# Kernel tuning notes

Hardware: AMD Instinct MI355X
Metric: run time of the kernel (lower is better)

Reference implementation:

```python
import jax, jax.numpy as jnp
import numpy as np

N, D, E, NNZ = 200000, 128, 1024, 1600000


def setup_inputs() -> dict:
    key = jax.random.key(0)
    ks = jax.random.split(key, 8)
    x = jax.random.normal(ks[0], (N, D), jnp.float32)
    tb_W = jax.random.normal(ks[1], (5, 3, D, D), jnp.float32) * 0.05
    tb_b = jax.random.normal(ks[2], (5, 3, D), jnp.float32) * 0.05
    hg_W = jax.random.normal(ks[3], (2, D, D), jnp.float32) * 0.05
    hg_b = jax.random.normal(ks[4], (2, D), jnp.float32) * 0.05
    hyperedge_attr = jax.random.normal(ks[5], (E, D), jnp.float32)
    node_idx = jax.random.randint(ks[6], (NNZ,), 0, N)
    edge_idx = jax.random.randint(ks[7], (NNZ,), 0, E)
    return dict(x=x, tb_W=tb_W, tb_b=tb_b, hg_W=hg_W, hg_b=hg_b,
                hyperedge_attr=hyperedge_attr, node_idx=node_idx,
                edge_idx=edge_idx, num_hyperedges=E)


def _time_block(x, W, b):
    # 1x1 Conv2d over channel dim == per-node linear. W:[3,D,D], b:[3,D]
    c1 = x @ W[0] + b[0]
    c2 = x @ W[1] + b[1]
    c3 = x @ W[2] + b[2]
    return jax.nn.relu(c1 + jax.nn.sigmoid(c2) + c3)


def _hypergraph_conv(x, node_idx, edge_idx, W, b, num_nodes, num_edges):
    # PyG HypergraphConv, use_attention=False (heads=1):
    # out = D^{-1} H B H^T (x W) + b, H given as COO (node_idx, edge_idx)
    xp = x @ W
    ones = jnp.ones(node_idx.shape[0], xp.dtype)
    Dn = jax.ops.segment_sum(ones, node_idx, num_segments=num_nodes)
    Dn = jnp.where(Dn > 0, 1.0 / Dn, 0.0)
    Be = jax.ops.segment_sum(ones, edge_idx, num_segments=num_edges)
    Be = jnp.where(Be > 0, 1.0 / Be, 0.0)
    # node -> hyperedge aggregation, normalized by 1/B_e
    m = jax.ops.segment_sum(xp[node_idx], edge_idx, num_segments=num_edges) * Be[:, None]
    # hyperedge -> node aggregation, normalized by 1/D_v
    out = jax.ops.segment_sum(m[edge_idx], node_idx, num_segments=num_nodes) * Dn[:, None]
    return out + b


def reference(x, tb_W, tb_b, hg_W, hg_b, hyperedge_attr, node_idx, edge_idx, num_hyperedges):
    # hyperedge_attr is unused when use_attention=False (faithful to PyG)
    n = x.shape[0]
    h = _time_block(x, tb_W[0], tb_b[0])
    h = _hypergraph_conv(h, node_idx, edge_idx, hg_W[0], hg_b[0], n, num_hyperedges)
    h = _time_block(h, tb_W[1], tb_b[1])
    h = _time_block(h, tb_W[2], tb_b[2])
    h = _hypergraph_conv(h, node_idx, edge_idx, hg_W[1], hg_b[1], n, num_hyperedges)
    h = _time_block(h, tb_W[3], tb_b[3])
    h = _time_block(h, tb_W[4], tb_b[4])
    return h
```

## Files before the change

kernel.cpp:

```cpp
#include <hip/hip_runtime.h>
#include <stdint.h>

#define N_NODES 200000
#define DIM     128
#define N_EDGES 1024
#define NNZ_C   1600000
#define NT64    3125

#define NBLK   250
#define CHUNK  6400
#define ITERS  25
#define NCB    196

#define NG_BLOCKS 2000
#define NG_WAVES  (NG_BLOCKS*4)
#define NG_K      25
#define NG_STAGE  512

typedef __attribute__((ext_vector_type(8))) short short8;
typedef __attribute__((ext_vector_type(4))) float f32x4;

__device__ __forceinline__ float u2f(uint32_t u){ union{uint32_t u;float f;} x; x.u=u; return x.f; }
__device__ __forceinline__ uint32_t f2u(float f){ union{uint32_t u;float f;} x; x.f=f; return x.u; }
__device__ __forceinline__ unsigned short f2bf(float f){
  uint32_t u = f2u(f);
  u += 0x7fffu + ((u >> 16) & 1u);
  return (unsigned short)(u >> 16);
}
__device__ __forceinline__ float fsig(float x){
  float e = __builtin_amdgcn_exp2f(x * -1.44269504088896340736f);
  return __builtin_amdgcn_rcpf(1.f + e);
}

__global__ void prep_tb_w(const float* __restrict__ W, short* __restrict__ Wt){
  int i = blockIdx.x*256 + threadIdx.x;
  if (i >= 5*256*128) return;
  int k   = i & 127;
  int col = (i >> 7) & 255;
  int s   = i >> 15;
  int j = col >> 7, n = col & 127;
  float v;
  if (j == 0)
    v = W[((s*3 + 0)*128 + k)*128 + n] + W[((s*3 + 2)*128 + k)*128 + n];
  else
    v = W[((s*3 + 1)*128 + k)*128 + n];
  Wt[i] = (short)f2bf(v);
}
__global__ void prep_hg_wf(const float* __restrict__ W, float* __restrict__ Wtf){
  int i = blockIdx.x*256 + threadIdx.x;
  if (i >= 2*128*128) return;
  int k = i & 127;
  int n = (i >> 7) & 127;
  int g = i >> 14;
  Wtf[i] = W[(g*128 + k)*128 + n];
}

__global__ __launch_bounds__(256) void hist_kernel(
    const int* __restrict__ nidx, const int* __restrict__ eidx,
    int* __restrict__ ebh, int* __restrict__ nbh)
{
  __shared__ int eh[N_EDGES];
  __shared__ int nh[NCB];
  int tid = threadIdx.x, blk = blockIdx.x;
  #pragma unroll
  for (int l = tid; l < N_EDGES; l += 256) eh[l] = 0;
  for (int l = tid; l < NCB; l += 256) nh[l] = 0;
  __syncthreads();
  int base = blk*CHUNK;
  for (int it = 0; it < ITERS; it++){
    int i = base + it*256 + tid;
    atomicAdd(&eh[eidx[i]], 1);
    atomicAdd(&nh[nidx[i] >> 10], 1);
  }
  __syncthreads();
  for (int l = tid; l < N_EDGES; l += 256) ebh[blk*N_EDGES + l] = eh[l];
  for (int l = tid; l < NCB; l += 256) nbh[blk*NCB + l] = nh[l];
}

__global__ __launch_bounds__(1024) void scan_kernel(
    int* __restrict__ ebh, int* __restrict__ eoff,
    int* __restrict__ nbh, int* __restrict__ cbase)
{
  __shared__ int sc[1024];
  int tid = threadIdx.x;
  if (blockIdx.x == 0){
    int e = tid;
    int total = 0;
    #pragma unroll 10
    for (int b = 0; b < NBLK; b++){
      int idx = b*N_EDGES + e;
      int t = ebh[idx];
      ebh[idx] = total;
      total += t;
    }
    sc[e] = total; __syncthreads();
    for (int off=1; off<1024; off<<=1){
      int v = (e >= off) ? sc[e-off] : 0;
      __syncthreads();
      sc[e] += v;
      __syncthreads();
    }
    int base = sc[e] - total;
    eoff[e] = base;
    if (e == 1023) eoff[1024] = sc[1023];
    #pragma unroll 10
    for (int b = 0; b < NBLK; b++) ebh[b*N_EDGES + e] += base;
  } else {
    int c = tid;
    int total = 0;
    if (c < NCB){
      #pragma unroll 10
      for (int b = 0; b < NBLK; b++){
        int idx = b*NCB + c;
        int t = nbh[idx];
        nbh[idx] = total;
        total += t;
      }
    }
    if (c < 256) sc[c] = (c < NCB) ? total : 0;
    __syncthreads();
    for (int off=1; off<256; off<<=1){
      int v = (c < 256 && c >= off) ? sc[c-off] : 0;
      __syncthreads();
      if (c < 256) sc[c] += v;
      __syncthreads();
    }
    if (c < NCB){
      int base = sc[c] - total;
      cbase[c] = base;
      if (c == NCB-1) cbase[NCB] = sc[c];
      #pragma unroll 10
      for (int b = 0; b < NBLK; b++) nbh[b*NCB + c] += base;
    }
  }
}

__global__ __launch_bounds__(256) void scatter_kernel(
    const int* __restrict__ nidx, const int* __restrict__ eidx,
    const int* __restrict__ ebh, const int* __restrict__ nbh,
    int* __restrict__ enodes, uint32_t* __restrict__ pairs)
{
  __shared__ int cure[N_EDGES];
  __shared__ int curn[NCB];
  int tid = threadIdx.x, blk = blockIdx.x;
  for (int l = tid; l < N_EDGES; l += 256) cure[l] = ebh[blk*N_EDGES + l];
  for (int l = tid; l < NCB; l += 256)     curn[l] = nbh[blk*NCB + l];
  __syncthreads();
  int base = blk*CHUNK;
  for (int it = 0; it < ITERS; it++){
    int i = base + it*256 + tid;
    int v = nidx[i], e = eidx[i];
    int pe = atomicAdd(&cure[e], 1);
    enodes[pe] = v;
    int pn = atomicAdd(&curn[v >> 10], 1);
    pairs[pn] = ((uint32_t)v << 10) | (uint32_t)e;
  }
}

__global__ __launch_bounds__(256) void node_build_kernel(
    const uint32_t* __restrict__ pairs, const int* __restrict__ cbase,
    int* __restrict__ noff, int* __restrict__ nedges)
{
  __shared__ int cnt[1024];
  __shared__ int off[1024];
  __shared__ int part[256];
  int tid = threadIdx.x, c = blockIdx.x;
  int n0 = c << 10;
  int nloc = min(1024, N_NODES - n0);
  int s = cbase[c], e = cbase[c+1];
  #pragma unroll
  for (int l = tid; l < 1024; l += 256) cnt[l] = 0;
  __syncthreads();
  for (int i = s + tid; i < e; i += 256)
    atomicAdd(&cnt[(pairs[i] >> 10) & 1023], 1);
  __syncthreads();
  int c0 = cnt[tid*4], c1 = cnt[tid*4+1], c2 = cnt[tid*4+2], c3 = cnt[tid*4+3];
  int sum = c0+c1+c2+c3;
  part[tid] = sum; __syncthreads();
  for (int o=1; o<256; o<<=1){
    int v = (tid >= o) ? part[tid-o] : 0;
    __syncthreads();
    part[tid] += v;
    __syncthreads();
  }
  int pb = part[tid] - sum;
  off[tid*4]   = pb;
  off[tid*4+1] = pb + c0;
  off[tid*4+2] = pb + c0 + c1;
  off[tid*4+3] = pb + c0 + c1 + c2;
  __syncthreads();
  for (int l = tid; l < nloc; l += 256) noff[n0 + l] = s + off[l];
  if (c == 0 && tid == 0) noff[N_NODES] = NNZ_C;
  __syncthreads();
  for (int i = s + tid; i < e; i += 256){
    uint32_t p = pairs[i];
    int local = (p >> 10) & 1023;
    int pos = s + atomicAdd(&off[local], 1);
    nedges[pos] = (int)((p & 1023) << 8);
  }
}

template<bool IN_F32, int OUT_MODE>
__global__ __launch_bounds__(512, 6) void gemm_kernel(
    const void* __restrict__ in, void* __restrict__ out,
    const short* __restrict__ Wt, const float* __restrict__ bias)
{
  __shared__ short Atile[2][64][136];
  const int tid  = threadIdx.x;
  const int lane = tid & 63;
  const int w    = tid >> 6;
  const int l15  = lane & 15;
  const int quad = lane >> 4;
  const int ncol = w*16 + l15;

  short8 bfrag[2][4];
  #pragma unroll
  for (int j = 0; j < 2; j++){
    const short* bp = Wt + (j*128 + ncol)*128 + quad*8;
    #pragma unroll
    for (int ks = 0; ks < 4; ks++)
      bfrag[j][ks] = *(const short8*)(bp + ks*32);
  }
  float bv13 = bias[ncol] + bias[256 + ncol];
  float bv2  = bias[128 + ncol];

  const int arow = tid >> 4;
  const int aseg = tid & 15;

  short8 pre0, pre1;
  auto loadA = [&](int t){
    int off0 = (t*64 + arow)*128 + aseg*8;
    int off1 = off0 + 32*128;
    if (IN_F32){
      const float* f = (const float*)in;
      #pragma unroll
      for (int h = 0; h < 2; h++){
        const float* fp = f + (h ? off1 : off0);
        f32x4 q0 = *(const f32x4*)fp;
        f32x4 q1 = *(const f32x4*)(fp + 4);
        short8 t0;
        #pragma unroll
        for (int u = 0; u < 4; u++){
          t0[u]   = (short)f2bf(q0[u]);
          t0[u+4] = (short)f2bf(q1[u]);
        }
        if (h) pre1 = t0; else pre0 = t0;
      }
    } else {
      pre0 = *(const short8*)((const short*)in + off0);
      pre1 = *(const short8*)((const short*)in + off1);
    }
  };

  int t = blockIdx.x;
  int p = 0;
  loadA(t);
  for (;;){
    *(short8*)&Atile[p][arow][aseg*8]      = pre0;
    *(short8*)&Atile[p][arow + 32][aseg*8] = pre1;
    __syncthreads();
    int tn = t + gridDim.x;
    if (tn < NT64) loadA(tn);

    const int base = t*64;
    #pragma unroll
    for (int rt = 0; rt < 4; rt++){
      short8 af[4];
      #pragma unroll
      for (int ks = 0; ks < 4; ks++)
        af[ks] = *(const short8*)&Atile[p][rt*16 + l15][ks*32 + quad*8];

      f32x4 acc[2];
      #pragma unroll
      for (int j = 0; j < 2; j++){
        acc[j] = (f32x4){0.f, 0.f, 0.f, 0.f};
        #pragma unroll
        for (int ks = 0; ks < 4; ks++)
          acc[j] = __builtin_amdgcn_mfma_f32_16x16x32_bf16(
              af[ks], bfrag[j][ks], acc[j], 0, 0, 0);
      }

      #pragma unroll
      for (int r = 0; r < 4; r++){
        int row = base + rt*16 + quad*4 + r;
        float sg = fsig(acc[1][r] + bv2);
        float v = acc[0][r] + bv13 + sg;
        v = fmaxf(v, 0.f);
        if (OUT_MODE == 1) ((float*)out)[row*128 + ncol] = v;
        else if (OUT_MODE == 0) ((unsigned short*)out)[row*128 + ncol] = f2bf(v);
        else {
          int pk = __builtin_amdgcn_cvt_pk_fp8_f32(v, v, 0, false);
          ((unsigned char*)out)[row*128 + ncol] = (unsigned char)(pk & 0xff);
        }
      }
    }
    if (tn >= NT64) break;
    t = tn;
    p ^= 1;
  }
}

__device__ __forceinline__ void acc16(float* a, uint4 r){
  uint32_t w[4] = {r.x, r.y, r.z, r.w};
  #pragma unroll
  for (int q = 0; q < 4; q++){
    auto lo = __builtin_amdgcn_cvt_pk_f32_fp8(w[q], false);
    auto hi = __builtin_amdgcn_cvt_pk_f32_fp8(w[q], true);
    a[q*4+0] += lo[0]; a[q*4+1] += lo[1]; a[q*4+2] += hi[0]; a[q*4+3] += hi[1];
  }
}

__global__ __launch_bounds__(256) void edge_gather_kernel(
    const unsigned char* __restrict__ h8, const int* __restrict__ eoff,
    const int* __restrict__ enodes, const float* __restrict__ Wtf,
    uint32_t* __restrict__ mbf)
{
  int e = blockIdx.x;
  int s = eoff[e], en = eoff[e+1];
  int tid  = threadIdx.x;
  int slot = tid >> 3;
  int ch   = tid & 7;
  const size_t choff = (size_t)ch * 16;

  float a[16];
  #pragma unroll
  for (int j = 0; j < 16; j++) a[j] = 0.f;

  int i0 = s + slot;
  int n0 = (i0      < en) ? enodes[i0]      : -1;
  int n1 = (i0 + 32 < en) ? enodes[i0 + 32] : -1;
  int n2 = (i0 + 64 < en) ? enodes[i0 + 64] : -1;
  int n3 = (i0 + 96 < en) ? enodes[i0 + 96] : -1;

  while (i0 < en){
    int i1 = i0 + 128;
    int m0 = (i1      < en) ? enodes[i1]      : -1;
    int m1 = (i1 + 32 < en) ? enodes[i1 + 32] : -1;
    int m2 = (i1 + 64 < en) ? enodes[i1 + 64] : -1;
    int m3 = (i1 + 96 < en) ? enodes[i1 + 96] : -1;

    uint4 r0 = *(const uint4*)(h8 + (((size_t)max(n0,0)) << 7) + choff);
    uint4 r1 = *(const uint4*)(h8 + (((size_t)max(n1,0)) << 7) + choff);
    uint4 r2 = *(const uint4*)(h8 + (((size_t)max(n2,0)) << 7) + choff);
    uint4 r3 = *(const uint4*)(h8 + (((size_t)max(n3,0)) << 7) + choff);
    if (n0 < 0) r0 = make_uint4(0,0,0,0);
    if (n1 < 0) r1 = make_uint4(0,0,0,0);
    if (n2 < 0) r2 = make_uint4(0,0,0,0);
    if (n3 < 0) r3 = make_uint4(0,0,0,0);

    acc16(a, r0); acc16(a, r1); acc16(a, r2); acc16(a, r3);

    n0 = m0; n1 = m1; n2 = m2; n3 = m3;
    i0 = i1;
  }

  __shared__ float red[32][132];
  __shared__ float srow[128];
  __shared__ float sacc[128];
  #pragma unroll
  for (int j = 0; j < 16; j++) red[slot][ch*16 + j] = a[j];
  __syncthreads();
  if (tid < 128){
    float sum = 0.f;
    #pragma unroll
    for (int r = 0; r < 32; r++) sum += red[r][tid];
    srow[tid] = sum;
  }
  __syncthreads();
  int deg = en - s;
  float be = deg > 0 ? 1.f/(float)deg : 0.f;
  if (tid < 128){
    const f32x4* w4 = (const f32x4*)(Wtf + tid*128);
    float acc = 0.f;
    #pragma unroll
    for (int k = 0; k < 32; k++){
      f32x4 qv = w4[k];
      acc += qv[0]*srow[k*4] + qv[1]*srow[k*4+1] + qv[2]*srow[k*4+2] + qv[3]*srow[k*4+3];
    }
    sacc[tid] = acc * be;
  }
  __syncthreads();
  if (tid < 64){
    uint32_t lo = f2bf(sacc[2*tid]);
    uint32_t hi = f2bf(sacc[2*tid+1]);
    mbf[e*64 + tid] = (hi << 16) | lo;
  }
}

__global__ __launch_bounds__(256) void node_gather_kernel(
    const uint32_t* __restrict__ mbf, const int* __restrict__ noff,
    const int* __restrict__ nedges, const float* __restrict__ hb,
    uint32_t* __restrict__ outp)
{
  __shared__ int sidx[4][NG_STAGE];
  const int wslot = threadIdx.x >> 6;
  const int wid   = (blockIdx.x << 2) | wslot;
  const int lane  = threadIdx.x & 63;
  const int lane4 = lane << 2;
  const float b0 = hb[2*lane], b1 = hb[2*lane+1];
  const int v0 = wid * NG_K;

  int eArr = noff[min(v0 + 1 + lane, N_NODES)];
  int sW   = __builtin_amdgcn_readfirstlane(noff[v0]);
  int send = __builtin_amdgcn_readlane(eArr, NG_K - 1);
  int n = send - sW;

  int* myIdx = sidx[wslot];
  bool useLds = (n <= NG_STAGE);
  if (useLds){
    for (int b = lane; b < n; b += 64) myIdx[b] = nedges[sW + b];
  }
  __syncthreads();

  const char* mb = (const char*)mbf;
  if (useLds){
    int s = sW;
    for (int vr = 0; vr < NG_K; vr++){
      int e = __builtin_amdgcn_readlane(eArr, vr);
      float a0 = 0.f, a1 = 0.f;
      uint32_t rlast = 0;
      for (int i = s; i < e; i += 8){
        uint32_t r[8];
        #pragma unroll
        for (int k = 0; k < 8; k++){
          int li = min(i + k, e - 1) - sW;
          r[k] = *(const uint32_t*)(mb + (myIdx[li] + lane4));
        }
        #pragma unroll
        for (int k = 0; k < 8; k++){
          a0 += u2f(r[k] << 16);
          a1 += u2f(r[k] & 0xffff0000u);
        }
        rlast = r[7];
      }
      int d = e - s;
      float dead = (float)(((d + 7) & ~7) - d);
      a0 -= dead * u2f(rlast << 16);
      a1 -= dead * u2f(rlast & 0xffff0000u);
      float dn = (d > 0) ? 1.f/(float)d : 0.f;
      uint32_t lo = f2bf(a0*dn + b0);
      uint32_t hi = f2bf(a1*dn + b1);
      outp[((size_t)(v0 + vr) << 6) | lane] = (hi << 16) | lo;
      s = e;
    }
  } else {
    int s = sW;
    for (int vr = 0; vr < NG_K; vr++){
      int e = __builtin_amdgcn_readlane(eArr, vr);
      float a0 = 0.f, a1 = 0.f;
      for (int i = s; i < e; i++){
        uint32_t r = *(const uint32_t*)(mb + (nedges[i] + lane4));
        a0 += u2f(r << 16);
        a1 += u2f(r & 0xffff0000u);
      }
      int d = e - s;
      float dn = (d > 0) ? 1.f/(float)d : 0.f;
      uint32_t lo = f2bf(a0*dn + b0);
      uint32_t hi = f2bf(a1*dn + b1);
      outp[((size_t)(v0 + vr) << 6) | lane] = (hi << 16) | lo;
      s = e;
    }
  }
}

extern "C" void kernel_launch(void* const* d_in, const int* in_sizes, int n_in,
                              void* d_out, int out_size, void* d_ws, size_t ws_size,
                              hipStream_t stream)
{
  (void)in_sizes; (void)n_in; (void)out_size; (void)ws_size;
  const float* x   = (const float*)d_in[0];
  const float* tbW = (const float*)d_in[1];
  const float* tbb = (const float*)d_in[2];
  const float* hgW = (const float*)d_in[3];
  const float* hgb = (const float*)d_in[4];
  const int* nidx  = (const int*)d_in[6];
  const int* eidx  = (const int*)d_in[7];
  float* out = (float*)d_out;

  char* p = (char*)d_ws;
  auto alloc = [&](size_t sz){ void* r = (void*)p; p += (sz + 255) & ~(size_t)255; return r; };
  unsigned short* hA = (unsigned short*)alloc((size_t)N_NODES*DIM*2);
  unsigned short* hB = (unsigned short*)alloc((size_t)N_NODES*DIM*2);
  unsigned char*  h8 = (unsigned char*)alloc((size_t)N_NODES*DIM);
  uint32_t* mbf = (uint32_t*)alloc((size_t)N_EDGES*64*4);
  short* WtTb = (short*)alloc((size_t)5*256*128*2);
  float* Wtf  = (float*)alloc((size_t)2*128*128*4);
  int* ebh  = (int*)alloc((size_t)NBLK*N_EDGES*4);
  int* nbh  = (int*)alloc((size_t)NBLK*NCB*4);
  int* eoff = (int*)alloc((N_EDGES+1)*4);
  int* cbase= (int*)alloc((NCB+1)*4);
  int* noff = (int*)alloc((size_t)(N_NODES+1)*4);
  int* enodes = (int*)alloc((size_t)NNZ_C*4);
  int* nedges = (int*)alloc((size_t)NNZ_C*4 + 64);
  uint32_t* pairs = (uint32_t*)h8;

  prep_tb_w<<<640, 256, 0, stream>>>(tbW, WtTb);
  prep_hg_wf<<<128, 256, 0, stream>>>(hgW, Wtf);

  hist_kernel<<<NBLK, 256, 0, stream>>>(nidx, eidx, ebh, nbh);
  scan_kernel<<<2, 1024, 0, stream>>>(ebh, eoff, nbh, cbase);
  scatter_kernel<<<NBLK, 256, 0, stream>>>(nidx, eidx, ebh, nbh, enodes, pairs);
  node_build_kernel<<<NCB, 256, 0, stream>>>(pairs, cbase, noff, nedges);

  gemm_kernel<true, 2><<<1250, 512, 0, stream>>>(x, h8, WtTb, tbb);
  edge_gather_kernel<<<N_EDGES, 256, 0, stream>>>(h8, eoff, enodes, Wtf, mbf);
  node_gather_kernel<<<NG_BLOCKS, 256, 0, stream>>>(mbf, noff, nedges, hgb, (uint32_t*)hA);
  gemm_kernel<false, 0><<<1250, 512, 0, stream>>>(hA, hB, WtTb + 1*32768, tbb + 1*384);
  gemm_kernel<false, 2><<<1250, 512, 0, stream>>>(hB, h8, WtTb + 2*32768, tbb + 2*384);
  edge_gather_kernel<<<N_EDGES, 256, 0, stream>>>(h8, eoff, enodes, Wtf + 16384, mbf);
  node_gather_kernel<<<NG_BLOCKS, 256, 0, stream>>>(mbf, noff, nedges, hgb + 128, (uint32_t*)hA);
  gemm_kernel<false, 0><<<1250, 512, 0, stream>>>(hA, hB, WtTb + 3*32768, tbb + 3*384);
  gemm_kernel<false, 1><<<1250, 512, 0, stream>>>(hB, out, WtTb + 4*32768, tbb + 4*384);
}
```

Measured before the change: 626.6 us.

## Overlap CSR construction with first GEMM on a second stream; single-buffer GEMM LDS

The hypergraph CSR build (hist, scan, scatter, node_build) moves onto a separate non-blocking stream, with events so it runs concurrently with weight prep and the first time-block GEMM. The pairs buffer gets its own allocation instead of aliasing h8, since the two now run at the same time. Separately, the GEMM's double-buffered A tile in LDS becomes a single buffer with an extra barrier, which reduces shared memory per block and may raise occupancy at the cost of more synchronisation. Concurrency depends on both streams finding free CUs.

```diff
diff --git a/kernel.cpp b/kernel.cpp
--- a/kernel.cpp
+++ b/kernel.cpp
@@ -205,7 +205,7 @@
     const void* __restrict__ in, void* __restrict__ out,
     const short* __restrict__ Wt, const float* __restrict__ bias)
 {
-  __shared__ short Atile[2][64][136];
+  __shared__ short Atile[64][136];
   const int tid  = threadIdx.x;
   const int lane = tid & 63;
   const int w    = tid >> 6;
@@ -253,11 +253,11 @@
   };
 
   int t = blockIdx.x;
-  int p = 0;
   loadA(t);
   for (;;){
-    *(short8*)&Atile[p][arow][aseg*8]      = pre0;
-    *(short8*)&Atile[p][arow + 32][aseg*8] = pre1;
+    __syncthreads();
+    *(short8*)&Atile[arow][aseg*8]      = pre0;
+    *(short8*)&Atile[arow + 32][aseg*8] = pre1;
     __syncthreads();
     int tn = t + gridDim.x;
     if (tn < NT64) loadA(tn);
@@ -268,7 +268,7 @@
       short8 af[4];
       #pragma unroll
       for (int ks = 0; ks < 4; ks++)
-        af[ks] = *(const short8*)&Atile[p][rt*16 + l15][ks*32 + quad*8];
+        af[ks] = *(const short8*)&Atile[rt*16 + l15][ks*32 + quad*8];
 
       f32x4 acc[2];
       #pragma unroll
@@ -296,7 +296,6 @@
     }
     if (tn >= NT64) break;
     t = tn;
-    p ^= 1;
   }
 }
 
@@ -492,17 +491,29 @@
   int* noff = (int*)alloc((size_t)(N_NODES+1)*4);
   int* enodes = (int*)alloc((size_t)NNZ_C*4);
   int* nedges = (int*)alloc((size_t)NNZ_C*4 + 64);
-  uint32_t* pairs = (uint32_t*)h8;
+  uint32_t* pairs = (uint32_t*)alloc((size_t)NNZ_C*4);
+
+  static hipStream_t s2 = nullptr;
+  static hipEvent_t evFork = nullptr, evCsr = nullptr;
+  if (!s2){
+    hipStreamCreateWithFlags(&s2, hipStreamNonBlocking);
+    hipEventCreateWithFlags(&evFork, hipEventDisableTiming);
+    hipEventCreateWithFlags(&evCsr, hipEventDisableTiming);
+  }
+
+  hipEventRecord(evFork, stream);
+  hipStreamWaitEvent(s2, evFork, 0);
+  hist_kernel<<<NBLK, 256, 0, s2>>>(nidx, eidx, ebh, nbh);
+  scan_kernel<<<2, 1024, 0, s2>>>(ebh, eoff, nbh, cbase);
+  scatter_kernel<<<NBLK, 256, 0, s2>>>(nidx, eidx, ebh, nbh, enodes, pairs);
+  node_build_kernel<<<NCB, 256, 0, s2>>>(pairs, cbase, noff, nedges);
+  hipEventRecord(evCsr, s2);
 
   prep_tb_w<<<640, 256, 0, stream>>>(tbW, WtTb);
   prep_hg_wf<<<128, 256, 0, stream>>>(hgW, Wtf);
-
-  hist_kernel<<<NBLK, 256, 0, stream>>>(nidx, eidx, ebh, nbh);
-  scan_kernel<<<2, 1024, 0, stream>>>(ebh, eoff, nbh, cbase);
-  scatter_kernel<<<NBLK, 256, 0, stream>>>(nidx, eidx, ebh, nbh, enodes, pairs);
-  node_build_kernel<<<NCB, 256, 0, stream>>>(pairs, cbase, noff, nedges);
-
   gemm_kernel<true, 2><<<1250, 512, 0, stream>>>(x, h8, WtTb, tbb);
+
+  hipStreamWaitEvent(stream, evCsr, 0);
   edge_gather_kernel<<<N_EDGES, 256, 0, stream>>>(h8, eoff, enodes, Wtf, mbf);
   node_gather_kernel<<<NG_BLOCKS, 256, 0, stream>>>(mbf, noff, nedges, hgb, (uint32_t*)hA);
   gemm_kernel<false, 0><<<1250, 512, 0, stream>>>(hA, hB, WtTb + 1*32768, tbb + 1*384);
```

Result: no change. 616.6 us (-1.6%).
